# Kernel optimization log

Measured on AMD Instinct MI355X. Metric: run time of the kernel, lower is better.

## Reference

```python
import jax, jax.numpy as jnp
import numpy as np

B, L, D, H = 32, 1024, 512, 512
ODE_STEPS = 6
DT = 1.0

def _unif(key, shape, fan_in):
    bound = 1.0 / np.sqrt(fan_in)
    return jax.random.uniform(key, shape, jnp.float32, -bound, bound)

def setup_inputs() -> dict:
    key = jax.random.key(0)
    ks = jax.random.split(key, 9)
    return {
        "x": jax.random.normal(ks[0], (B, L, D), jnp.float32),
        "log_tau": jnp.zeros((H,), jnp.float32),
        "W_in": _unif(ks[1], (H, D), D),
        "b_in": _unif(ks[2], (H,), D),
        "W_rec": _unif(ks[3], (H, H), H),
        "W_gate": _unif(ks[4], (H, D + H), D + H),
        "b_gate": _unif(ks[5], (H,), D + H),
        "W_out": _unif(ks[6], (H, H), H),
        "b_out": _unif(ks[7], (H,), H),
    }

def reference(x, log_tau, W_in, b_in, W_rec, W_gate, b_gate, W_out, b_out):
    Bx, Lx, Dx = x.shape
    Hx = log_tau.shape[0]
    tau = jnp.exp(log_tau)                      # (H,)
    sub_dt = DT / ODE_STEPS
    # Split gate weight: cat([x, h]) @ W_gate.T == x @ Wg_x.T + h @ Wg_h.T
    Wg_x, Wg_h = W_gate[:, :Dx], W_gate[:, Dx:]
    # Precompute input-dependent drives for the whole sequence (time-parallel GEMMs)
    drive = jnp.einsum('bld,hd->blh', x, W_in) + b_in      # W_in(x), (B,L,H)
    gate_x = jnp.einsum('bld,hd->blh', x, Wg_x) + b_gate   # input part of gate pre-act

    def step(h, inp):
        d, gx = inp  # (B,H) each
        for _ in range(ODE_STEPS):  # small fixed unroll of ODE sub-steps
            rec = h @ W_rec.T
            gate = jax.nn.sigmoid(gx + h @ Wg_h.T)
            f = -h + gate * jnp.tanh(d + rec)
            h = h + (sub_dt / tau) * f
        return h, h

    h0 = jnp.zeros((Bx, Hx), x.dtype)
    h_last, fwd = jax.lax.scan(step, h0, (drive.transpose(1, 0, 2), gate_x.transpose(1, 0, 2)))
    fwd = fwd.transpose(1, 0, 2)                 # (B,L,H)
    output = fwd @ W_out.T + b_out               # output_proj; dropout is identity (p=0)
    return output, h_last
```

## Files before the change

### kernel.cpp

```cpp
#include <hip/hip_runtime.h>

typedef unsigned short u16;
typedef unsigned int   u32;
typedef unsigned long long u64;

#define LTC_B 32
#define LTC_L 1024
#define LTC_D 512
#define LTC_H 512
#define NG 8
#define NP 16
#define NBG 4

typedef _Float16 f16x8  __attribute__((ext_vector_type(8)));
typedef _Float16 f16x2t __attribute__((ext_vector_type(2)));
typedef float    f32x4  __attribute__((ext_vector_type(4)));

static __device__ __forceinline__ u32 packh(float a, float b) {
    f16x2t p; p[0] = (_Float16)a; p[1] = (_Float16)b;
    return __builtin_bit_cast(u32, p);
}
static __device__ __forceinline__ float unplo(u32 w) {
    return (float)__builtin_bit_cast(f16x2t, w)[0];
}
static __device__ __forceinline__ float unphi(u32 w) {
    return (float)__builtin_bit_cast(f16x2t, w)[1];
}
static __device__ __forceinline__ float sigm(float x) {
    return 1.f / (1.f + __expf(-x));
}
static __device__ __forceinline__ float tanh_f(float x) {
    float e = __expf(2.f * x);
    return 1.f - 2.f / (e + 1.f);
}
static __device__ __forceinline__ f16x8 cvt8(const float* p) {
    const float4 a = *(const float4*)p;
    const float4 b = *(const float4*)(p + 4);
    f16x8 r;
    r[0] = (_Float16)a.x; r[1] = (_Float16)a.y; r[2] = (_Float16)a.z; r[3] = (_Float16)a.w;
    r[4] = (_Float16)b.x; r[5] = (_Float16)b.y; r[6] = (_Float16)b.z; r[7] = (_Float16)b.w;
    return r;
}
static __device__ __forceinline__ bool stamp2(u64 a, u64 b, u32 k) {
    return ((u32)(a >> 32) == k) & ((u32)(b >> 32) == k);
}

__global__ __launch_bounds__(256) void gemm_a32_c16(
    const float* __restrict__ A, const float* __restrict__ W, int ldb,
    const float* __restrict__ bias, u16* __restrict__ C)
{
    const int wave = threadIdx.x >> 6;
    const int lane = threadIdx.x & 63;
    const int tile = blockIdx.x * 4 + wave;
    const int nt = tile & 7;
    const int mt = tile >> 3;
    const int r16 = lane & 15;
    const int kq  = (lane >> 4) * 8;

    const float* ap = A + (size_t)(mt * 64 + r16) * LTC_D + kq;
    const float* wp = W + (size_t)(nt * 64 + r16) * ldb + kq;

    f32x4 acc[4][4];
    #pragma unroll
    for (int i = 0; i < 4; ++i)
        #pragma unroll
        for (int jj = 0; jj < 4; ++jj) acc[i][jj] = (f32x4){0.f, 0.f, 0.f, 0.f};

    for (int ks = 0; ks < 16; ++ks) {
        f16x8 af[4], bf[4];
        #pragma unroll
        for (int t = 0; t < 4; ++t) {
            af[t] = cvt8(ap + (size_t)t * 16 * LTC_D + ks * 32);
            bf[t] = cvt8(wp + (size_t)t * 16 * ldb  + ks * 32);
        }
        #pragma unroll
        for (int mi = 0; mi < 4; ++mi)
            #pragma unroll
            for (int ni = 0; ni < 4; ++ni)
                acc[mi][ni] = __builtin_amdgcn_mfma_f32_16x16x32_f16(
                    af[mi], bf[ni], acc[mi][ni], 0, 0, 0);
    }
    const int row = (lane >> 4) * 4;
    const int col = lane & 15;
    #pragma unroll
    for (int ni = 0; ni < 4; ++ni) {
        const int n = nt * 64 + ni * 16 + col;
        const float bv = bias[n];
        #pragma unroll
        for (int mi = 0; mi < 4; ++mi)
            #pragma unroll
            for (int r = 0; r < 4; ++r) {
                _Float16 h = (_Float16)(acc[mi][ni][r] + bv);
                C[(size_t)(mt * 64 + mi * 16 + row + r) * LTC_H + n] =
                    __builtin_bit_cast(u16, h);
            }
    }
}

__global__ __launch_bounds__(256) void gemm_a16_c32(
    const u16* __restrict__ A, const float* __restrict__ W,
    const float* __restrict__ bias, float* __restrict__ C)
{
    const int wave = threadIdx.x >> 6;
    const int lane = threadIdx.x & 63;
    const int tile = blockIdx.x * 4 + wave;
    const int nt = tile & 7;
    const int mt = tile >> 3;
    const int r16 = lane & 15;
    const int kq  = (lane >> 4) * 8;

    const _Float16* ap = (const _Float16*)A + (size_t)(mt * 64 + r16) * LTC_D + kq;
    const float*    wp = W + (size_t)(nt * 64 + r16) * LTC_H + kq;

    f32x4 acc[4][4];
    #pragma unroll
    for (int i = 0; i < 4; ++i)
        #pragma unroll
        for (int jj = 0; jj < 4; ++jj) acc[i][jj] = (f32x4){0.f, 0.f, 0.f, 0.f};

    for (int ks = 0; ks < 16; ++ks) {
        f16x8 af[4], bf[4];
        #pragma unroll
        for (int t = 0; t < 4; ++t) {
            af[t] = *(const f16x8*)(ap + (size_t)t * 16 * LTC_D + ks * 32);
            bf[t] = cvt8(wp + (size_t)t * 16 * LTC_H + ks * 32);
        }
        #pragma unroll
        for (int mi = 0; mi < 4; ++mi)
            #pragma unroll
            for (int ni = 0; ni < 4; ++ni)
                acc[mi][ni] = __builtin_amdgcn_mfma_f32_16x16x32_f16(
                    af[mi], bf[ni], acc[mi][ni], 0, 0, 0);
    }
    const int row = (lane >> 4) * 4;
    const int col = lane & 15;
    #pragma unroll
    for (int ni = 0; ni < 4; ++ni) {
        const int n = nt * 64 + ni * 16 + col;
        const float bv = bias[n];
        #pragma unroll
        for (int mi = 0; mi < 4; ++mi)
            #pragma unroll
            for (int r = 0; r < 4; ++r)
                C[(size_t)(mt * 64 + mi * 16 + row + r) * LTC_H + n] =
                    acc[mi][ni][r] + bv;
    }
}

__global__ __launch_bounds__(256) void ltc_scan(
    u32* __restrict__ drive,
    const u32* __restrict__ gatex,
    const float* __restrict__ W_rec,
    const float* __restrict__ W_gate,
    const float* __restrict__ log_tau,
    u64* __restrict__ hbuf,
    float* __restrict__ hlast)
{
    const int g   = blockIdx.x & 7;
    const int p   = blockIdx.x >> 3;
    const int tid = threadIdx.x;
    const int lane = tid & 63;
    const int wv   = tid >> 6;

    __shared__ u32 hTu[16][260];
    __shared__ float red2[2][64][17];

    const int nl = wv * 16 + (lane & 15);
    const int kq = (lane >> 4) * 8;
    const float* wrow = (nl < 32)
        ? (W_rec  + (size_t)(32 * p + nl) * LTC_H)
        : (W_gate + (size_t)(32 * p + nl - 32) * (LTC_D + LTC_H) + LTC_D);
    f16x8 Wf[16];
    #pragma unroll
    for (int ks = 0; ks < 16; ++ks) Wf[ks] = cvt8(wrow + ks * 32 + kq);

    for (int i = tid; i < 16 * 260; i += 256) (&hTu[0][0])[i] = 0;

    const int ub = tid >> 4;
    const int jp = tid & 15;
    const int j0 = 32 * p + 2 * jp;
    const int gb = g * NBG + ub;
    float h0 = 0.f, h1 = 0.f, stau0 = 0.f, stau1 = 0.f;
    size_t dwofs = 0;
    if (tid < 64) {
        stau0 = (1.f / 6.f) * __expf(-log_tau[j0]);
        stau1 = (1.f / 6.f) * __expf(-log_tau[j0 + 1]);
        dwofs = (size_t)gb * LTC_L * 256 + 16 * p + jp;
        __hip_atomic_store(hbuf + (size_t)g * (NBG * 256) + (size_t)ub * 256
                               + 16 * p + jp,
                           0ull, __ATOMIC_RELAXED, __HIP_MEMORY_SCOPE_AGENT);
    }
    __syncthreads();

    const _Float16* hrow = (const _Float16*)&hTu[lane & 15][0];
    const int redn = wv * 16 + (lane & 15);
    const int redb = (lane >> 4) * 4;
    u32 kp1 = 0;
    int budget = 1 << 22;
    const bool own = ((tid >> 4) == p);

    u32 dw = 0, gw = 0;
    if (tid < 64) { dw = drive[dwofs]; gw = gatex[dwofs]; }

    for (int l = 0; l < LTC_L; ++l) {
        const float d0 = unplo(dw), d1 = unphi(dw);
        const float gx0 = unplo(gw), gx1 = unphi(gw);
        u32 dn = 0, gn = 0;
        if (tid < 64 && l + 1 < LTC_L) {
            dn = drive[dwofs + (size_t)(l + 1) * 256];
            gn = gatex[dwofs + (size_t)(l + 1) * 256];
        }
        #pragma unroll 1
        for (int s = 0; s < 6; ++s) {
            const u32 kold = kp1, knew = kp1 + 1;
            const size_t pbOld = (size_t)((kold & 1u) * NG + g) * (NBG * 256);
            const size_t pbNew = (size_t)((knew & 1u) * NG + g) * (NBG * 256);
            const u64* sbO = hbuf + pbOld + tid;
            const u64* sbN = hbuf + pbNew + tid;

            u64 y0 = 0, y1 = 0;
            if (!own) {
                y0 = __hip_atomic_load(sbO + 512, __ATOMIC_RELAXED,
                                       __HIP_MEMORY_SCOPE_AGENT);
                y1 = __hip_atomic_load(sbO + 768, __ATOMIC_RELAXED,
                                       __HIP_MEMORY_SCOPE_AGENT);
            }
            {
                f32x4 acc0 = (f32x4){0.f, 0.f, 0.f, 0.f}, acc1 = acc0;
                #pragma unroll
                for (int ks = 0; ks < 16; ks += 2) {
                    const f16x8 a0 = *(const f16x8*)(hrow + ks * 32 + kq);
                    const f16x8 a1 = *(const f16x8*)(hrow + (ks + 1) * 32 + kq);
                    acc0 = __builtin_amdgcn_mfma_f32_16x16x32_f16(a0, Wf[ks],     acc0, 0, 0, 0);
                    acc1 = __builtin_amdgcn_mfma_f32_16x16x32_f16(a1, Wf[ks + 1], acc1, 0, 0, 0);
                }
                #pragma unroll
                for (int r = 0; r < 4; ++r) red2[0][redn][redb + r] = acc0[r] + acc1[r];
            }
            if (!own) {
                while (!stamp2(y0, y1, kold) && --budget > 0) {
                    y0 = __hip_atomic_load(sbO + 512, __ATOMIC_RELAXED,
                                           __HIP_MEMORY_SCOPE_AGENT);
                    y1 = __hip_atomic_load(sbO + 768, __ATOMIC_RELAXED,
                                           __HIP_MEMORY_SCOPE_AGENT);
                }
                hTu[2][tid] = (u32)y0;
                hTu[3][tid] = (u32)y1;
            }
            __syncthreads();

            if (tid < 32) {
                const float rec0 = red2[0][2 * jp][ub],     gh0 = red2[0][32 + 2 * jp][ub];
                const float rec1 = red2[0][2 * jp + 1][ub], gh1 = red2[0][32 + 2 * jp + 1][ub];
                h0 += stau0 * (sigm(gx0 + gh0) * tanh_f(d0 + rec0) - h0);
                h1 += stau1 * (sigm(gx1 + gh1) * tanh_f(d1 + rec1) - h1);
                const u32 pr = packh(h0, h1);
                hTu[ub][16 * p + jp] = pr;
                __hip_atomic_store(hbuf + pbNew + (size_t)ub * 256 + 16 * p + jp,
                                   ((u64)knew << 32) | (u64)pr,
                                   __ATOMIC_RELAXED, __HIP_MEMORY_SCOPE_AGENT);
            }
            {
                f32x4 acc0 = (f32x4){0.f, 0.f, 0.f, 0.f}, acc1 = acc0;
                #pragma unroll
                for (int ks = 0; ks < 16; ks += 2) {
                    const f16x8 a0 = *(const f16x8*)(hrow + ks * 32 + kq);
                    const f16x8 a1 = *(const f16x8*)(hrow + (ks + 1) * 32 + kq);
                    acc0 = __builtin_amdgcn_mfma_f32_16x16x32_f16(a0, Wf[ks],     acc0, 0, 0, 0);
                    acc1 = __builtin_amdgcn_mfma_f32_16x16x32_f16(a1, Wf[ks + 1], acc1, 0, 0, 0);
                }
                #pragma unroll
                for (int r = 0; r < 4; ++r) red2[1][redn][redb + r] = acc0[r] + acc1[r];
            }
            __syncthreads();

            u64 x0 = 0, x1 = 0;
            if (!own) {
                x0 = __hip_atomic_load(sbN,       __ATOMIC_RELAXED,
                                       __HIP_MEMORY_SCOPE_AGENT);
                x1 = __hip_atomic_load(sbN + 256, __ATOMIC_RELAXED,
                                       __HIP_MEMORY_SCOPE_AGENT);
            }
            if (tid >= 32 && tid < 64) {
                const float rec0 = red2[1][2 * jp][ub],     gh0 = red2[1][32 + 2 * jp][ub];
                const float rec1 = red2[1][2 * jp + 1][ub], gh1 = red2[1][32 + 2 * jp + 1][ub];
                h0 += stau0 * (sigm(gx0 + gh0) * tanh_f(d0 + rec0) - h0);
                h1 += stau1 * (sigm(gx1 + gh1) * tanh_f(d1 + rec1) - h1);
                const u32 pr = packh(h0, h1);
                hTu[ub][16 * p + jp] = pr;
                __hip_atomic_store(hbuf + pbNew + (size_t)ub * 256 + 16 * p + jp,
                                   ((u64)knew << 32) | (u64)pr,
                                   __ATOMIC_RELAXED, __HIP_MEMORY_SCOPE_AGENT);
            }
            if (!own) {
                while (!stamp2(x0, x1, knew) && --budget > 0) {
                    x0 = __hip_atomic_load(sbN,       __ATOMIC_RELAXED,
                                           __HIP_MEMORY_SCOPE_AGENT);
                    x1 = __hip_atomic_load(sbN + 256, __ATOMIC_RELAXED,
                                           __HIP_MEMORY_SCOPE_AGENT);
                }
                hTu[0][tid] = (u32)x0;
                hTu[1][tid] = (u32)x1;
            }
            __syncthreads();
            kp1 = knew;
        }
        if (tid < 64) drive[dwofs + (size_t)l * 256] = packh(h0, h1);
        dw = dn; gw = gn;
    }
    if (tid < 64) {
        hlast[(size_t)gb * LTC_H + j0]     = h0;
        hlast[(size_t)gb * LTC_H + j0 + 1] = h1;
    }
}

extern "C" void kernel_launch(void* const* d_in, const int* in_sizes, int n_in,
                              void* d_out, int out_size, void* d_ws, size_t ws_size,
                              hipStream_t stream)
{
    const float* x       = (const float*)d_in[0];
    const float* log_tau = (const float*)d_in[1];
    const float* W_in    = (const float*)d_in[2];
    const float* b_in    = (const float*)d_in[3];
    const float* W_rec   = (const float*)d_in[4];
    const float* W_gate  = (const float*)d_in[5];
    const float* b_gate  = (const float*)d_in[6];
    const float* W_out   = (const float*)d_in[7];
    const float* b_out   = (const float*)d_in[8];

    float* out   = (float*)d_out;
    float* hlast = out + (size_t)LTC_B * LTC_L * LTC_H;

    u32* ws    = (u32*)d_ws;
    u32* drive = ws;
    u32* gatex = ws + 8388608;
    u64* hbuf  = (u64*)(ws + 16777216);

    const int blocks = (LTC_B * LTC_L / 64) * (LTC_H / 64) / 4;

    gemm_a32_c16<<<blocks, 256, 0, stream>>>(x, W_in, LTC_D, b_in, (u16*)drive);
    gemm_a32_c16<<<blocks, 256, 0, stream>>>(x, W_gate, LTC_D + LTC_H, b_gate, (u16*)gatex);
    ltc_scan<<<NG * NP, 256, 0, stream>>>(drive, gatex, W_rec, W_gate, log_tau,
                                          hbuf, hlast);
    gemm_a16_c32<<<blocks, 256, 0, stream>>>((const u16*)drive, W_out, b_out, out);
}
```

Baseline: 10.39 ms.

## Use 128-bit coherent loads for peer state and overlap half-batch update with MFMA

Peer hidden-state polling now uses inline-asm global_load_dwordx4 with sc0 sc1 (cache-bypassing) instead of pairs of 64-bit atomic loads. Each thread fetches two adjacent stamped entries in one request, and the thread-to-data mapping is reworked so 128 threads per row cover the exchange. The first half-batch ODE update and its publish are moved inside the second MFMA block, so the gate math overlaps the matrix work. The aim is fewer memory transactions on the critical cross-block sync path and less serial latency per sub-step. In exchange it relies on hand-written asm and explicit vmcnt waits for ordering.

```diff
diff --git a/kernel.cpp b/kernel.cpp
--- a/kernel.cpp
+++ b/kernel.cpp
@@ -15,6 +15,7 @@
 typedef _Float16 f16x8  __attribute__((ext_vector_type(8)));
 typedef _Float16 f16x2t __attribute__((ext_vector_type(2)));
 typedef float    f32x4  __attribute__((ext_vector_type(4)));
+typedef u32      u32x4v __attribute__((ext_vector_type(4)));
 
 static __device__ __forceinline__ u32 packh(float a, float b) {
     f16x2t p; p[0] = (_Float16)a; p[1] = (_Float16)b;
@@ -41,8 +42,14 @@
     r[4] = (_Float16)b.x; r[5] = (_Float16)b.y; r[6] = (_Float16)b.z; r[7] = (_Float16)b.w;
     return r;
 }
-static __device__ __forceinline__ bool stamp2(u64 a, u64 b, u32 k) {
-    return ((u32)(a >> 32) == k) & ((u32)(b >> 32) == k);
+static __device__ __forceinline__ u32x4v gld_issue(const u64* p) {
+    u32x4v r;
+    asm volatile("global_load_dwordx4 %0, %1, off sc0 sc1"
+                 : "=v"(r) : "v"((u64)p) : "memory");
+    return r;
+}
+static __device__ __forceinline__ void gld_wait(u32x4v& r) {
+    asm volatile("s_waitcnt vmcnt(0)" : "+v"(r) : : "memory");
 }
 
 __global__ __launch_bounds__(256) void gemm_a32_c16(
@@ -197,7 +204,11 @@
     const int redb = (lane >> 4) * 4;
     u32 kp1 = 0;
     int budget = 1 << 22;
-    const bool own = ((tid >> 4) == p);
+
+    const int gh   = tid & 127;
+    const int grow = tid >> 7;
+    const int gc0  = 2 * gh;
+    const bool gskip = (gh >> 3) == p;
 
     u32 dw = 0, gw = 0;
     if (tid < 64) { dw = drive[dwofs]; gw = gatex[dwofs]; }
@@ -215,16 +226,10 @@
             const u32 kold = kp1, knew = kp1 + 1;
             const size_t pbOld = (size_t)((kold & 1u) * NG + g) * (NBG * 256);
             const size_t pbNew = (size_t)((knew & 1u) * NG + g) * (NBG * 256);
-            const u64* sbO = hbuf + pbOld + tid;
-            const u64* sbN = hbuf + pbNew + tid;
-
-            u64 y0 = 0, y1 = 0;
-            if (!own) {
-                y0 = __hip_atomic_load(sbO + 512, __ATOMIC_RELAXED,
-                                       __HIP_MEMORY_SCOPE_AGENT);
-                y1 = __hip_atomic_load(sbO + 768, __ATOMIC_RELAXED,
-                                       __HIP_MEMORY_SCOPE_AGENT);
-            }
+
+            const u64* gpY = hbuf + pbOld + 512 + (size_t)grow * 256 + gc0;
+            u32x4v gy = {0, 0, 0, 0};
+            if (!gskip) gy = gld_issue(gpY);
             {
                 f32x4 acc0 = (f32x4){0.f, 0.f, 0.f, 0.f}, acc1 = acc0;
                 #pragma unroll
@@ -237,29 +242,16 @@
                 #pragma unroll
                 for (int r = 0; r < 4; ++r) red2[0][redn][redb + r] = acc0[r] + acc1[r];
             }
-            if (!own) {
-                while (!stamp2(y0, y1, kold) && --budget > 0) {
-                    y0 = __hip_atomic_load(sbO + 512, __ATOMIC_RELAXED,
-                                           __HIP_MEMORY_SCOPE_AGENT);
-                    y1 = __hip_atomic_load(sbO + 768, __ATOMIC_RELAXED,
-                                           __HIP_MEMORY_SCOPE_AGENT);
-                }
-                hTu[2][tid] = (u32)y0;
-                hTu[3][tid] = (u32)y1;
+            if (!gskip) {
+                gld_wait(gy);
+                while (!((gy[1] == kold) & (gy[3] == kold)) && --budget > 0) {
+                    gy = gld_issue(gpY); gld_wait(gy);
+                }
+                hTu[2 + grow][gc0]     = gy[0];
+                hTu[2 + grow][gc0 + 1] = gy[2];
             }
             __syncthreads();
 
-            if (tid < 32) {
-                const float rec0 = red2[0][2 * jp][ub],     gh0 = red2[0][32 + 2 * jp][ub];
-                const float rec1 = red2[0][2 * jp + 1][ub], gh1 = red2[0][32 + 2 * jp + 1][ub];
-                h0 += stau0 * (sigm(gx0 + gh0) * tanh_f(d0 + rec0) - h0);
-                h1 += stau1 * (sigm(gx1 + gh1) * tanh_f(d1 + rec1) - h1);
-                const u32 pr = packh(h0, h1);
-                hTu[ub][16 * p + jp] = pr;
-                __hip_atomic_store(hbuf + pbNew + (size_t)ub * 256 + 16 * p + jp,
-                                   ((u64)knew << 32) | (u64)pr,
-                                   __ATOMIC_RELAXED, __HIP_MEMORY_SCOPE_AGENT);
-            }
             {
                 f32x4 acc0 = (f32x4){0.f, 0.f, 0.f, 0.f}, acc1 = acc0;
                 #pragma unroll
@@ -269,18 +261,25 @@
                     acc0 = __builtin_amdgcn_mfma_f32_16x16x32_f16(a0, Wf[ks],     acc0, 0, 0, 0);
                     acc1 = __builtin_amdgcn_mfma_f32_16x16x32_f16(a1, Wf[ks + 1], acc1, 0, 0, 0);
                 }
+                if (tid < 32) {
+                    const float rec0 = red2[0][2 * jp][ub],     gh0 = red2[0][32 + 2 * jp][ub];
+                    const float rec1 = red2[0][2 * jp + 1][ub], gh1 = red2[0][32 + 2 * jp + 1][ub];
+                    h0 += stau0 * (sigm(gx0 + gh0) * tanh_f(d0 + rec0) - h0);
+                    h1 += stau1 * (sigm(gx1 + gh1) * tanh_f(d1 + rec1) - h1);
+                    const u32 pr = packh(h0, h1);
+                    hTu[ub][16 * p + jp] = pr;
+                    __hip_atomic_store(hbuf + pbNew + (size_t)ub * 256 + 16 * p + jp,
+                                       ((u64)knew << 32) | (u64)pr,
+                                       __ATOMIC_RELAXED, __HIP_MEMORY_SCOPE_AGENT);
+                }
                 #pragma unroll
                 for (int r = 0; r < 4; ++r) red2[1][redn][redb + r] = acc0[r] + acc1[r];
             }
             __syncthreads();
 
-            u64 x0 = 0, x1 = 0;
-            if (!own) {
-                x0 = __hip_atomic_load(sbN,       __ATOMIC_RELAXED,
-                                       __HIP_MEMORY_SCOPE_AGENT);
-                x1 = __hip_atomic_load(sbN + 256, __ATOMIC_RELAXED,
-                                       __HIP_MEMORY_SCOPE_AGENT);
-            }
+            const u64* gpX = hbuf + pbNew + (size_t)grow * 256 + gc0;
+            u32x4v gx = {0, 0, 0, 0};
+            if (!gskip) gx = gld_issue(gpX);
             if (tid >= 32 && tid < 64) {
                 const float rec0 = red2[1][2 * jp][ub],     gh0 = red2[1][32 + 2 * jp][ub];
                 const float rec1 = red2[1][2 * jp + 1][ub], gh1 = red2[1][32 + 2 * jp + 1][ub];
@@ -292,15 +291,13 @@
                                    ((u64)knew << 32) | (u64)pr,
                                    __ATOMIC_RELAXED, __HIP_MEMORY_SCOPE_AGENT);
             }
-            if (!own) {
-                while (!stamp2(x0, x1, knew) && --budget > 0) {
-                    x0 = __hip_atomic_load(sbN,       __ATOMIC_RELAXED,
-                                           __HIP_MEMORY_SCOPE_AGENT);
-                    x1 = __hip_atomic_load(sbN + 256, __ATOMIC_RELAXED,
-                                           __HIP_MEMORY_SCOPE_AGENT);
-                }
-                hTu[0][tid] = (u32)x0;
-                hTu[1][tid] = (u32)x1;
+            if (!gskip) {
+                gld_wait(gx);
+                while (!((gx[1] == knew) & (gx[3] == knew)) && --budget > 0) {
+                    gx = gld_issue(gpX); gld_wait(gx);
+                }
+                hTu[grow][gc0]     = gx[0];
+                hTu[grow][gc0 + 1] = gx[2];
             }
             __syncthreads();
             kp1 = knew;
```

After: 10.48 ms. Within noise of the previous version (+0.9%).

## Specialize scan waves: MFMA waves separate from update and spin-poll waves

Applied to the files above, without the earlier changes.

The scan block doubles to 512 threads. Waves 0-3 now do only the recurrent MFMA work. Wave 4 runs the elementwise ODE update and publishes h, and waves 4-7 poll the cross-block exchange buffer. Taking the global spin-waits and activation math off the MFMA waves is meant to let the matvec for one batch half overlap with the update and polling for the other. The cost is more threads per block, higher register pressure from launch bounds of 512, and reordered hTu writes, which need careful sync reasoning.

```diff
diff --git a/kernel.cpp b/kernel.cpp
--- a/kernel.cpp
+++ b/kernel.cpp
@@ -43,6 +43,10 @@
 }
 static __device__ __forceinline__ bool stamp2(u64 a, u64 b, u32 k) {
     return ((u32)(a >> 32) == k) & ((u32)(b >> 32) == k);
+}
+static __device__ __forceinline__ bool stamp4(u64 a, u64 b, u64 c, u64 d, u32 k) {
+    return ((u32)(a >> 32) == k) & ((u32)(b >> 32) == k) &
+           ((u32)(c >> 32) == k) & ((u32)(d >> 32) == k);
 }
 
 __global__ __launch_bounds__(256) void gemm_a32_c16(
@@ -147,7 +151,7 @@
     }
 }
 
-__global__ __launch_bounds__(256) void ltc_scan(
+__global__ __launch_bounds__(512) void ltc_scan(
     u32* __restrict__ drive,
     const u32* __restrict__ gatex,
     const float* __restrict__ W_rec,
@@ -165,24 +169,29 @@
     __shared__ u32 hTu[16][260];
     __shared__ float red2[2][64][17];
 
-    const int nl = wv * 16 + (lane & 15);
     const int kq = (lane >> 4) * 8;
-    const float* wrow = (nl < 32)
-        ? (W_rec  + (size_t)(32 * p + nl) * LTC_H)
-        : (W_gate + (size_t)(32 * p + nl - 32) * (LTC_D + LTC_H) + LTC_D);
+
     f16x8 Wf[16];
-    #pragma unroll
-    for (int ks = 0; ks < 16; ++ks) Wf[ks] = cvt8(wrow + ks * 32 + kq);
-
-    for (int i = tid; i < 16 * 260; i += 256) (&hTu[0][0])[i] = 0;
-
-    const int ub = tid >> 4;
-    const int jp = tid & 15;
+    if (wv < 4) {
+        const int nl = wv * 16 + (lane & 15);
+        const float* wrow = (nl < 32)
+            ? (W_rec  + (size_t)(32 * p + nl) * LTC_H)
+            : (W_gate + (size_t)(32 * p + nl - 32) * (LTC_D + LTC_H) + LTC_D);
+        #pragma unroll
+        for (int ks = 0; ks < 16; ++ks) Wf[ks] = cvt8(wrow + ks * 32 + kq);
+    }
+
+    for (int i = tid; i < 16 * 260; i += 512) (&hTu[0][0])[i] = 0;
+
+    const int ut = tid - 256;
+    const bool isupd = (ut >= 0) && (ut < 64);
+    const int ub = ut >> 4;
+    const int jp = ut & 15;
     const int j0 = 32 * p + 2 * jp;
     const int gb = g * NBG + ub;
     float h0 = 0.f, h1 = 0.f, stau0 = 0.f, stau1 = 0.f;
     size_t dwofs = 0;
-    if (tid < 64) {
+    if (isupd) {
         stau0 = (1.f / 6.f) * __expf(-log_tau[j0]);
         stau1 = (1.f / 6.f) * __expf(-log_tau[j0 + 1]);
         dwofs = (size_t)gb * LTC_L * 256 + 16 * p + jp;
@@ -193,20 +202,24 @@
     __syncthreads();
 
     const _Float16* hrow = (const _Float16*)&hTu[lane & 15][0];
-    const int redn = wv * 16 + (lane & 15);
+    const int redn = (wv & 3) * 16 + (lane & 15);
     const int redb = (lane >> 4) * 4;
     u32 kp1 = 0;
     int budget = 1 << 22;
-    const bool own = ((tid >> 4) == p);
+
+    const int qA = tid - 256;
+    const bool skipA = ((qA >> 4) == p);
+    const int qC = tid - 384;
+    const bool skipC = ((qC >> 3) == p);
 
     u32 dw = 0, gw = 0;
-    if (tid < 64) { dw = drive[dwofs]; gw = gatex[dwofs]; }
+    if (isupd) { dw = drive[dwofs]; gw = gatex[dwofs]; }
 
     for (int l = 0; l < LTC_L; ++l) {
         const float d0 = unplo(dw), d1 = unphi(dw);
         const float gx0 = unplo(gw), gx1 = unphi(gw);
         u32 dn = 0, gn = 0;
-        if (tid < 64 && l + 1 < LTC_L) {
+        if (isupd && l + 1 < LTC_L) {
             dn = drive[dwofs + (size_t)(l + 1) * 256];
             gn = gatex[dwofs + (size_t)(l + 1) * 256];
         }
@@ -215,17 +228,8 @@
             const u32 kold = kp1, knew = kp1 + 1;
             const size_t pbOld = (size_t)((kold & 1u) * NG + g) * (NBG * 256);
             const size_t pbNew = (size_t)((knew & 1u) * NG + g) * (NBG * 256);
-            const u64* sbO = hbuf + pbOld + tid;
-            const u64* sbN = hbuf + pbNew + tid;
-
-            u64 y0 = 0, y1 = 0;
-            if (!own) {
-                y0 = __hip_atomic_load(sbO + 512, __ATOMIC_RELAXED,
-                                       __HIP_MEMORY_SCOPE_AGENT);
-                y1 = __hip_atomic_load(sbO + 768, __ATOMIC_RELAXED,
-                                       __HIP_MEMORY_SCOPE_AGENT);
-            }
-            {
+
+            if (wv < 4) {
                 f32x4 acc0 = (f32x4){0.f, 0.f, 0.f, 0.f}, acc1 = acc0;
                 #pragma unroll
                 for (int ks = 0; ks < 16; ks += 2) {
@@ -236,31 +240,25 @@
                 }
                 #pragma unroll
                 for (int r = 0; r < 4; ++r) red2[0][redn][redb + r] = acc0[r] + acc1[r];
-            }
-            if (!own) {
-                while (!stamp2(y0, y1, kold) && --budget > 0) {
-                    y0 = __hip_atomic_load(sbO + 512, __ATOMIC_RELAXED,
-                                           __HIP_MEMORY_SCOPE_AGENT);
-                    y1 = __hip_atomic_load(sbO + 768, __ATOMIC_RELAXED,
+            } else if (!skipA) {
+                const u64* s2 = hbuf + pbOld + 512 + qA;
+                const u64* s3 = hbuf + pbOld + 768 + qA;
+                u64 a2 = __hip_atomic_load(s2, __ATOMIC_RELAXED,
+                                           __HIP_MEMORY_SCOPE_AGENT);
+                u64 a3 = __hip_atomic_load(s3, __ATOMIC_RELAXED,
+                                           __HIP_MEMORY_SCOPE_AGENT);
+                while (!stamp2(a2, a3, kold) && --budget > 0) {
+                    a2 = __hip_atomic_load(s2, __ATOMIC_RELAXED,
+                                           __HIP_MEMORY_SCOPE_AGENT);
+                    a3 = __hip_atomic_load(s3, __ATOMIC_RELAXED,
                                            __HIP_MEMORY_SCOPE_AGENT);
                 }
-                hTu[2][tid] = (u32)y0;
-                hTu[3][tid] = (u32)y1;
+                hTu[2][qA] = (u32)a2;
+                hTu[3][qA] = (u32)a3;
             }
             __syncthreads();
 
-            if (tid < 32) {
-                const float rec0 = red2[0][2 * jp][ub],     gh0 = red2[0][32 + 2 * jp][ub];
-                const float rec1 = red2[0][2 * jp + 1][ub], gh1 = red2[0][32 + 2 * jp + 1][ub];
-                h0 += stau0 * (sigm(gx0 + gh0) * tanh_f(d0 + rec0) - h0);
-                h1 += stau1 * (sigm(gx1 + gh1) * tanh_f(d1 + rec1) - h1);
-                const u32 pr = packh(h0, h1);
-                hTu[ub][16 * p + jp] = pr;
-                __hip_atomic_store(hbuf + pbNew + (size_t)ub * 256 + 16 * p + jp,
-                                   ((u64)knew << 32) | (u64)pr,
-                                   __ATOMIC_RELAXED, __HIP_MEMORY_SCOPE_AGENT);
-            }
-            {
+            if (wv < 4) {
                 f32x4 acc0 = (f32x4){0.f, 0.f, 0.f, 0.f}, acc1 = acc0;
                 #pragma unroll
                 for (int ks = 0; ks < 16; ks += 2) {
@@ -271,44 +269,62 @@
                 }
                 #pragma unroll
                 for (int r = 0; r < 4; ++r) red2[1][redn][redb + r] = acc0[r] + acc1[r];
+            } else if (ut < 32) {
+                const float rec0 = red2[0][2 * jp][ub],     gh0 = red2[0][32 + 2 * jp][ub];
+                const float rec1 = red2[0][2 * jp + 1][ub], gh1 = red2[0][32 + 2 * jp + 1][ub];
+                h0 += stau0 * (sigm(gx0 + gh0) * tanh_f(d0 + rec0) - h0);
+                h1 += stau1 * (sigm(gx1 + gh1) * tanh_f(d1 + rec1) - h1);
+                const u32 pr = packh(h0, h1);
+                __hip_atomic_store(hbuf + pbNew + (size_t)ub * 256 + 16 * p + jp,
+                                   ((u64)knew << 32) | (u64)pr,
+                                   __ATOMIC_RELAXED, __HIP_MEMORY_SCOPE_AGENT);
+                hTu[ub][16 * p + jp] = pr;
             }
             __syncthreads();
 
-            u64 x0 = 0, x1 = 0;
-            if (!own) {
-                x0 = __hip_atomic_load(sbN,       __ATOMIC_RELAXED,
-                                       __HIP_MEMORY_SCOPE_AGENT);
-                x1 = __hip_atomic_load(sbN + 256, __ATOMIC_RELAXED,
-                                       __HIP_MEMORY_SCOPE_AGENT);
-            }
-            if (tid >= 32 && tid < 64) {
+            if (ut >= 32 && ut < 64) {
                 const float rec0 = red2[1][2 * jp][ub],     gh0 = red2[1][32 + 2 * jp][ub];
                 const float rec1 = red2[1][2 * jp + 1][ub], gh1 = red2[1][32 + 2 * jp + 1][ub];
                 h0 += stau0 * (sigm(gx0 + gh0) * tanh_f(d0 + rec0) - h0);
                 h1 += stau1 * (sigm(gx1 + gh1) * tanh_f(d1 + rec1) - h1);
                 const u32 pr = packh(h0, h1);
-                hTu[ub][16 * p + jp] = pr;
                 __hip_atomic_store(hbuf + pbNew + (size_t)ub * 256 + 16 * p + jp,
                                    ((u64)knew << 32) | (u64)pr,
                                    __ATOMIC_RELAXED, __HIP_MEMORY_SCOPE_AGENT);
-            }
-            if (!own) {
-                while (!stamp2(x0, x1, knew) && --budget > 0) {
-                    x0 = __hip_atomic_load(sbN,       __ATOMIC_RELAXED,
-                                           __HIP_MEMORY_SCOPE_AGENT);
-                    x1 = __hip_atomic_load(sbN + 256, __ATOMIC_RELAXED,
+                hTu[ub][16 * p + jp] = pr;
+            } else if (wv >= 6 && !skipC) {
+                const int c0 = 2 * qC, c1 = c0 + 1;
+                const u64* b0 = hbuf + pbNew;
+                u64 a0 = __hip_atomic_load(b0 + c0,       __ATOMIC_RELAXED,
+                                           __HIP_MEMORY_SCOPE_AGENT);
+                u64 a1 = __hip_atomic_load(b0 + c1,       __ATOMIC_RELAXED,
+                                           __HIP_MEMORY_SCOPE_AGENT);
+                u64 a2 = __hip_atomic_load(b0 + 256 + c0, __ATOMIC_RELAXED,
+                                           __HIP_MEMORY_SCOPE_AGENT);
+                u64 a3 = __hip_atomic_load(b0 + 256 + c1, __ATOMIC_RELAXED,
+                                           __HIP_MEMORY_SCOPE_AGENT);
+                while (!stamp4(a0, a1, a2, a3, knew) && --budget > 0) {
+                    a0 = __hip_atomic_load(b0 + c0,       __ATOMIC_RELAXED,
+                                           __HIP_MEMORY_SCOPE_AGENT);
+                    a1 = __hip_atomic_load(b0 + c1,       __ATOMIC_RELAXED,
+                                           __HIP_MEMORY_SCOPE_AGENT);
+                    a2 = __hip_atomic_load(b0 + 256 + c0, __ATOMIC_RELAXED,
+                                           __HIP_MEMORY_SCOPE_AGENT);
+                    a3 = __hip_atomic_load(b0 + 256 + c1, __ATOMIC_RELAXED,
                                            __HIP_MEMORY_SCOPE_AGENT);
                 }
-                hTu[0][tid] = (u32)x0;
-                hTu[1][tid] = (u32)x1;
+                hTu[0][c0] = (u32)a0;
+                hTu[0][c1] = (u32)a1;
+                hTu[1][c0] = (u32)a2;
+                hTu[1][c1] = (u32)a3;
             }
             __syncthreads();
             kp1 = knew;
         }
-        if (tid < 64) drive[dwofs + (size_t)l * 256] = packh(h0, h1);
+        if (isupd) drive[dwofs + (size_t)l * 256] = packh(h0, h1);
         dw = dn; gw = gn;
     }
-    if (tid < 64) {
+    if (isupd) {
         hlast[(size_t)gb * LTC_H + j0]     = h0;
         hlast[(size_t)gb * LTC_H + j0 + 1] = h1;
     }
@@ -340,7 +356,7 @@
 
     gemm_a32_c16<<<blocks, 256, 0, stream>>>(x, W_in, LTC_D, b_in, (u16*)drive);
     gemm_a32_c16<<<blocks, 256, 0, stream>>>(x, W_gate, LTC_D + LTC_H, b_gate, (u16*)gatex);
-    ltc_scan<<<NG * NP, 256, 0, stream>>>(drive, gatex, W_rec, W_gate, log_tau,
+    ltc_scan<<<NG * NP, 512, 0, stream>>>(drive, gatex, W_rec, W_gate, log_tau,
                                           hbuf, hlast);
     gemm_a16_c32<<<blocks, 256, 0, stream>>>((const u16*)drive, W_out, b_out, out);
 }
```

Result: faster. 9.021 ms (-13.2%).
